# Optimization experiments

Measured on AMD Instinct MI355X. Metric: run time of the kernel, lower is better.

Reference implementation:

```python
import jax, jax.numpy as jnp
import numpy as np

HIDDEN = 1024


def setup_inputs() -> dict:
    key = jax.random.key(0)
    ks = jax.random.split(key, 9)
    B, S, Kq, H = 16, 4096, 64, HIDDEN
    scale = 1.0 / np.sqrt(H)
    return {
        "queries": jax.random.normal(ks[0], (B, Kq, H), jnp.float32),
        "keys": jax.random.normal(ks[1], (B, S, H), jnp.float32),
        "values": jax.random.normal(ks[2], (B, S, H), jnp.float32),
        "Wq": jax.random.normal(ks[3], (H, H), jnp.float32) * scale,
        "bq": jax.random.normal(ks[4], (H,), jnp.float32) * 0.02,
        "Wk": jax.random.normal(ks[5], (H, H), jnp.float32) * scale,
        "bk": jax.random.normal(ks[6], (H,), jnp.float32) * 0.02,
        "Wv": jax.random.normal(ks[7], (H, H), jnp.float32) * scale,
        "bv": jax.random.normal(ks[8], (H,), jnp.float32) * 0.02,
    }


def reference(queries, keys, values, Wq, bq, Wk, bk, Wv, bv):
    H = Wq.shape[0]
    scaling = jax.lax.rsqrt(jnp.asarray(H, queries.dtype))
    # torch Linear: x @ W^T + b
    q = queries @ Wq.T + bq            # (B, Kq, H)
    k = keys @ Wk.T + bk               # (B, S, H)
    v = values @ Wv.T + bv             # (B, S, H)
    # scores: k @ q^T -> (B, S, Kq), softmax over seq_len axis (dim=1)
    scores = jnp.einsum('bsh,bqh->bsq', k, q) * scaling
    attention_weights = jax.nn.softmax(scores, axis=1)
    # context: attn^T @ v -> (B, Kq, H)
    context = jnp.einsum('bsq,bsh->bqh', attention_weights, v)
    return context, attention_weights
```

## Files before the change

kernel.cpp:

```cpp
#include <hip/hip_runtime.h>
#include <hip/hip_bf16.h>

#define H 1024
#define SEQ 4096
#define BQ 64
#define NB 16

typedef float f32x4 __attribute__((ext_vector_type(4)));
typedef __bf16 bf16x8 __attribute__((ext_vector_type(8)));

__device__ __forceinline__ void split_bf16(const float* x, bf16x8& hi, bf16x8& lo)
{
    #pragma unroll
    for (int i = 0; i < 8; ++i) {
        float v = x[i];
        __bf16 h = (__bf16)v;
        hi[i] = h;
        lo[i] = (__bf16)(v - (float)h);
    }
}

__device__ __forceinline__ void gload_lds16(const float* g, void* lds)
{
    __builtin_amdgcn_global_load_lds(
        (const __attribute__((address_space(1))) void*)g,
        (__attribute__((address_space(3))) void*)lds, 16, 0, 0);
}

template<bool CVEC>
__global__ __launch_bounds__(512)
void gemm_bt_512(const float* __restrict__ A, const float* __restrict__ Bm,
                 const float* __restrict__ bias, float* __restrict__ C,
                 float scale, const float* __restrict__ bk,
                 float* __restrict__ cvec, float cscale)
{
    const int m0 = blockIdx.x * 64;
    const int n0 = blockIdx.y * 64;
    const int t   = threadIdx.x;
    const int w   = t >> 6;
    const int wm  = w & 3;
    const int kh  = w >> 2;
    const int l   = t & 63;
    const int row = l & 15;
    const int kg  = l >> 4;

    const float* ap = A + (size_t)(m0 + wm * 16 + row) * H + kh * 512 + kg * 8;
    const float* bp = Bm + (size_t)(n0 + row) * H + kh * 512 + kg * 8;

    f32x4 acc[4] = {};
    for (int k0 = 0; k0 < 512; k0 += 32) {
        float a8[8];
        *reinterpret_cast<float4*>(&a8[0]) = *reinterpret_cast<const float4*>(ap + k0);
        *reinterpret_cast<float4*>(&a8[4]) = *reinterpret_cast<const float4*>(ap + k0 + 4);
        bf16x8 ahi, alo;
        split_bf16(a8, ahi, alo);
        #pragma unroll
        for (int j = 0; j < 4; ++j) {
            float b8[8];
            const float* bjp = bp + (size_t)j * 16 * H + k0;
            *reinterpret_cast<float4*>(&b8[0]) = *reinterpret_cast<const float4*>(bjp);
            *reinterpret_cast<float4*>(&b8[4]) = *reinterpret_cast<const float4*>(bjp + 4);
            bf16x8 bhi, blo;
            split_bf16(b8, bhi, blo);
            acc[j] = __builtin_amdgcn_mfma_f32_16x16x32_bf16(ahi, bhi, acc[j], 0, 0, 0);
            acc[j] = __builtin_amdgcn_mfma_f32_16x16x32_bf16(ahi, blo, acc[j], 0, 0, 0);
            acc[j] = __builtin_amdgcn_mfma_f32_16x16x32_bf16(alo, bhi, acc[j], 0, 0, 0);
        }
    }

    __shared__ f32x4 red[4][4][64];
    if (kh == 1) {
        #pragma unroll
        for (int j = 0; j < 4; ++j) red[wm][j][l] = acc[j];
    }
    __syncthreads();
    if (kh == 0) {
        float p[4] = {0.f, 0.f, 0.f, 0.f};
        #pragma unroll
        for (int j = 0; j < 4; ++j) {
            f32x4 s = acc[j] + red[wm][j][l];
            int n = n0 + j * 16 + row;
            float bb = bias ? bias[n] : 0.f;
            float bkv = CVEC ? bk[n] : 0.f;
            #pragma unroll
            for (int r = 0; r < 4; ++r) {
                int m = m0 + wm * 16 + kg * 4 + r;
                float o = s[r] * scale + bb;
                C[(size_t)m * H + n] = o;
                if (CVEC) p[r] += o * bkv;
            }
        }
        if (CVEC) {
            #pragma unroll
            for (int r = 0; r < 4; ++r) {
                #pragma unroll
                for (int off = 1; off < 16; off <<= 1)
                    p[r] += __shfl_xor(p[r], off);
            }
            if (row == 0) {
                #pragma unroll
                for (int r = 0; r < 4; ++r)
                    atomicAdd(&cvec[m0 + wm * 16 + kg * 4 + r], p[r] * cscale);
            }
        }
    }
}

__global__ __launch_bounds__(512)
void ngemm_direct(const float* __restrict__ A, const float* __restrict__ Wk,
                  __bf16* __restrict__ Nhi, __bf16* __restrict__ Nlo, float scale)
{
    const int m0 = blockIdx.x * 64;
    const int n0 = blockIdx.y * 64;
    const int t   = threadIdx.x;
    const int w   = t >> 6;
    const int wm  = w & 3;
    const int kh  = w >> 2;
    const int l   = t & 63;
    const int row = l & 15;
    const int kg  = l >> 4;

    const float* ap = A + (size_t)(m0 + wm * 16 + row) * H + kh * 512 + kg * 8;
    const float* bp = Wk + (size_t)(kh * 512 + kg * 8) * H + n0 + row;

    f32x4 acc[4] = {};
    for (int k0 = 0; k0 < 512; k0 += 32) {
        float a8[8];
        *reinterpret_cast<float4*>(&a8[0]) = *reinterpret_cast<const float4*>(ap + k0);
        *reinterpret_cast<float4*>(&a8[4]) = *reinterpret_cast<const float4*>(ap + k0 + 4);
        bf16x8 ahi, alo;
        split_bf16(a8, ahi, alo);
        #pragma unroll
        for (int j = 0; j < 4; ++j) {
            float b8[8];
            #pragma unroll
            for (int e = 0; e < 8; ++e)
                b8[e] = bp[(size_t)(k0 + e) * H + j * 16];
            bf16x8 bhi, blo;
            split_bf16(b8, bhi, blo);
            acc[j] = __builtin_amdgcn_mfma_f32_16x16x32_bf16(ahi, bhi, acc[j], 0, 0, 0);
            acc[j] = __builtin_amdgcn_mfma_f32_16x16x32_bf16(ahi, blo, acc[j], 0, 0, 0);
            acc[j] = __builtin_amdgcn_mfma_f32_16x16x32_bf16(alo, bhi, acc[j], 0, 0, 0);
        }
    }

    __shared__ f32x4 red[4][4][64];
    if (kh == 1) {
        #pragma unroll
        for (int j = 0; j < 4; ++j) red[wm][j][l] = acc[j];
    }
    __syncthreads();
    if (kh == 0) {
        #pragma unroll
        for (int j = 0; j < 4; ++j) {
            f32x4 s = acc[j] + red[wm][j][l];
            int n = n0 + j * 16 + row;
            #pragma unroll
            for (int r = 0; r < 4; ++r) {
                int m = m0 + wm * 16 + kg * 4 + r;
                float v = s[r] * scale;
                __bf16 hi = (__bf16)v;
                Nhi[(size_t)m * H + n] = hi;
                Nlo[(size_t)m * H + n] = (__bf16)(v - (float)hi);
            }
        }
    }
}

__global__ __launch_bounds__(512, 4)
void scores_mfma(const float* __restrict__ keys,
                 const __bf16* __restrict__ Nhi, const __bf16* __restrict__ Nlo,
                 const float* __restrict__ cvec, float* __restrict__ scores,
                 float* __restrict__ pmax, float* __restrict__ psum)
{
    const int id = blockIdx.x;
    const int x  = id & 7;
    const int m  = id >> 3;
    const int b  = 2 * x + (m >> 5);
    const int ch = m & 31;
    const int s0 = ch * 128;

    const int t   = threadIdx.x;
    const int w   = t >> 6;
    const int l   = t & 63;
    const int row = l & 15;
    const int kg  = l >> 4;

    __shared__ __bf16 nshH[2][64][8][8];
    __shared__ __bf16 nshL[2][64][8][8];
    __shared__ float redm[8][64];

    const float* ka = keys + ((size_t)b * SEQ + s0 + w * 16 + row) * H + kg * 8;
    const __bf16* nhb = Nhi + (size_t)b * BQ * H;
    const __bf16* nlb = Nlo + (size_t)b * BQ * H;

    const int sqi = t >> 3;
    const int skb = t & 7;
    const int ssl = skb ^ (sqi & 7);

    float4 kr[2][4];
    bf16x8 nh[2], nl[2];
    #pragma unroll
    for (int ii = 0; ii < 2; ++ii) {
        kr[0][2 * ii + 0] = *reinterpret_cast<const float4*>(ka + ii * 32);
        kr[0][2 * ii + 1] = *reinterpret_cast<const float4*>(ka + ii * 32 + 4);
    }
    {
        size_t go = (size_t)sqi * H + skb * 8;
        nh[0] = *reinterpret_cast<const bf16x8*>(nhb + go);
        nl[0] = *reinterpret_cast<const bf16x8*>(nlb + go);
    }

    f32x4 acc[4] = {};
    #pragma unroll
    for (int c = 0; c < 16; ++c) {
        const int buf = c & 1;
        *reinterpret_cast<bf16x8*>(&nshH[buf][sqi][ssl][0]) = nh[buf];
        *reinterpret_cast<bf16x8*>(&nshL[buf][sqi][ssl][0]) = nl[buf];
        __syncthreads();
        if (c < 15) {
            const int kc = (c + 1) * 64;
            #pragma unroll
            for (int ii = 0; ii < 2; ++ii) {
                kr[buf ^ 1][2 * ii + 0] = *reinterpret_cast<const float4*>(ka + kc + ii * 32);
                kr[buf ^ 1][2 * ii + 1] = *reinterpret_cast<const float4*>(ka + kc + ii * 32 + 4);
            }
            size_t go = (size_t)sqi * H + kc + skb * 8;
            nh[buf ^ 1] = *reinterpret_cast<const bf16x8*>(nhb + go);
            nl[buf ^ 1] = *reinterpret_cast<const bf16x8*>(nlb + go);
        }
        #pragma unroll
        for (int ii = 0; ii < 2; ++ii) {
            float a8[8];
            *reinterpret_cast<float4*>(&a8[0]) = kr[buf][2 * ii + 0];
            *reinterpret_cast<float4*>(&a8[4]) = kr[buf][2 * ii + 1];
            bf16x8 ahi, alo;
            split_bf16(a8, ahi, alo);
            const int kb = ii * 4 + kg;
            const int slot = kb ^ (row & 7);
            #pragma unroll
            for (int j = 0; j < 4; ++j) {
                const int qi = j * 16 + row;
                bf16x8 bhi = *reinterpret_cast<const bf16x8*>(&nshH[buf][qi][slot][0]);
                bf16x8 blo = *reinterpret_cast<const bf16x8*>(&nshL[buf][qi][slot][0]);
                acc[j] = __builtin_amdgcn_mfma_f32_16x16x32_bf16(ahi, bhi, acc[j], 0, 0, 0);
                acc[j] = __builtin_amdgcn_mfma_f32_16x16x32_bf16(ahi, blo, acc[j], 0, 0, 0);
                acc[j] = __builtin_amdgcn_mfma_f32_16x16x32_bf16(alo, bhi, acc[j], 0, 0, 0);
            }
        }
    }

    #pragma unroll
    for (int j = 0; j < 4; ++j) {
        int qi = j * 16 + row;
        float cv = cvec[b * BQ + qi];
        #pragma unroll
        for (int r = 0; r < 4; ++r) {
            acc[j][r] += cv;
            int s = s0 + w * 16 + kg * 4 + r;
            scores[((size_t)b * SEQ + s) * BQ + qi] = acc[j][r];
        }
    }
    float mj[4];
    #pragma unroll
    for (int j = 0; j < 4; ++j) {
        float mm = fmaxf(fmaxf(acc[j][0], acc[j][1]), fmaxf(acc[j][2], acc[j][3]));
        mm = fmaxf(mm, __shfl_xor(mm, 16));
        mm = fmaxf(mm, __shfl_xor(mm, 32));
        mj[j] = mm;
    }
    __syncthreads();
    if (kg == 0) {
        #pragma unroll
        for (int j = 0; j < 4; ++j) redm[w][j * 16 + row] = mj[j];
    }
    __syncthreads();
    float Mj[4];
    #pragma unroll
    for (int j = 0; j < 4; ++j) {
        const int qi = j * 16 + row;
        float M = redm[0][qi];
        #pragma unroll
        for (int ww = 1; ww < 8; ++ww) M = fmaxf(M, redm[ww][qi]);
        Mj[j] = M;
    }
    float sj[4];
    #pragma unroll
    for (int j = 0; j < 4; ++j) {
        float s = 0.f;
        #pragma unroll
        for (int r = 0; r < 4; ++r) s += __expf(acc[j][r] - Mj[j]);
        s += __shfl_xor(s, 16);
        s += __shfl_xor(s, 32);
        sj[j] = s;
    }
    __syncthreads();
    if (kg == 0) {
        #pragma unroll
        for (int j = 0; j < 4; ++j) redm[w][j * 16 + row] = sj[j];
    }
    __syncthreads();
    if (w == 0 && kg == 0) {
        #pragma unroll
        for (int j = 0; j < 4; ++j) {
            const int qi = j * 16 + row;
            float ss = 0.f;
            #pragma unroll
            for (int ww = 0; ww < 8; ++ww) ss += redm[ww][qi];
            pmax[((size_t)b * 32 + ch) * 64 + qi] = Mj[j];
            psum[((size_t)b * 32 + ch) * 64 + qi] = ss;
        }
    }
}

__global__ __launch_bounds__(256)
void sm_norm(float* __restrict__ attn, const float* __restrict__ pmax,
             const float* __restrict__ psum, __hip_bfloat16* __restrict__ abfT)
{
    __shared__ float tile[64][133];
    const int b  = blockIdx.y;
    const int ch = blockIdx.x;
    const int t  = threadIdx.x;
    const int qi = t & 63;
    const int g  = t >> 6;

    float M = -1e30f;
    #pragma unroll 4
    for (int c = 0; c < 32; ++c)
        M = fmaxf(M, pmax[((size_t)b * 32 + c) * 64 + qi]);
    float ssum = 0.f;
    #pragma unroll 4
    for (int c = 0; c < 32; ++c)
        ssum += psum[((size_t)b * 32 + c) * 64 + qi] *
                __expf(pmax[((size_t)b * 32 + c) * 64 + qi] - M);
    const float inv = 1.f / ssum;

    float* sb = attn + ((size_t)b * SEQ + ch * 128) * BQ;
    #pragma unroll 8
    for (int i = 0; i < 32; ++i) {
        int sl = g + i * 4;
        size_t idx = (size_t)sl * BQ + qi;
        float w = __expf(sb[idx] - M) * inv;
        sb[idx] = w;
        tile[qi][sl] = w;
    }
    __syncthreads();
    const int qo = t >> 2;
    const int c  = (t & 3) * 32;
    __hip_bfloat16* dst = abfT + ((size_t)(b * BQ + qo)) * SEQ + ch * 128 + c;
    #pragma unroll
    for (int v = 0; v < 4; ++v) {
        bf16x8 w8;
        #pragma unroll
        for (int e = 0; e < 8; ++e)
            w8[e] = (__bf16)tile[qo][c + v * 8 + e];
        *reinterpret_cast<bf16x8*>(dst + v * 8) = w8;
    }
}

template<int SC>
__global__ __launch_bounds__(256)
void tmat_mfma(const __hip_bfloat16* __restrict__ abfT,
               const float* __restrict__ values,
               float* __restrict__ Tpart)
{
    const int i  = blockIdx.x;
    const int h0 = ((i >> 3) & 7) * 128;
    const int g  = (i & 7) + 8 * (i >> 6);
    const int b  = g / SC;
    const int sc = g % SC;
    const int schunk = SEQ / SC;

    const int w   = threadIdx.x >> 6;
    const int l   = threadIdx.x & 63;
    const int row = l & 15;
    const int kg  = l >> 4;
    const int sbase = sc * schunk;

    __shared__ float vlds[2][32][128];

    const __hip_bfloat16* ap = abfT + ((size_t)b * BQ + row) * SEQ + sbase + kg * 8;
    const float* vb = values + ((size_t)b * SEQ + sbase) * H + h0;

    const int nk = schunk / 32;

    #define STAGE(buf, k0)                                                     \
        {                                                                      \
            _Pragma("unroll")                                                  \
            for (int ii = 0; ii < 4; ++ii) {                                   \
                int elem = w * 1024 + ii * 256 + l * 4;                        \
                int k    = elem >> 7;                                          \
                int cc   = elem & 127;                                         \
                int csw  = cc ^ ((k >> 3) << 4);                               \
                const float* src = vb + (size_t)((k0) + k) * H + csw;          \
                gload_lds16(src, (void*)(&vlds[buf][0][0] + w * 1024 + ii * 256)); \
            }                                                                  \
        }

    f32x4 acc[4][2] = {};
    STAGE(0, 0);
    __syncthreads();

    for (int ks = 0; ks < nk; ++ks) {
        const int buf = ks & 1;
        if (ks + 1 < nk) STAGE(buf ^ 1, (ks + 1) * 32);
        const int k0 = ks * 32;
        bf16x8 a[4];
        #pragma unroll
        for (int q = 0; q < 4; ++q)
            a[q] = *reinterpret_cast<const bf16x8*>(ap + (size_t)q * 16 * SEQ + k0);
        #pragma unroll
        for (int j = 0; j < 2; ++j) {
            const int col = (w * 32 + j * 16 + row) ^ (kg << 4);
            float b8[8];
            #pragma unroll
            for (int e = 0; e < 8; ++e)
                b8[e] = vlds[buf][kg * 8 + e][col];
            bf16x8 bhi, blo;
            split_bf16(b8, bhi, blo);
            #pragma unroll
            for (int q = 0; q < 4; ++q) {
                acc[q][j] = __builtin_amdgcn_mfma_f32_16x16x32_bf16(a[q], bhi, acc[q][j], 0, 0, 0);
                acc[q][j] = __builtin_amdgcn_mfma_f32_16x16x32_bf16(a[q], blo, acc[q][j], 0, 0, 0);
            }
        }
        __syncthreads();
    }
    #undef STAGE

    float* tp = Tpart + ((size_t)sc * NB + b) * BQ * H;
    #pragma unroll
    for (int q = 0; q < 4; ++q) {
        #pragma unroll
        for (int j = 0; j < 2; ++j) {
            int h = h0 + w * 32 + j * 16 + row;
            #pragma unroll
            for (int r = 0; r < 4; ++r) {
                int qi = q * 16 + kg * 4 + r;
                tp[(size_t)qi * H + h] = acc[q][j][r];
            }
        }
    }
}

template<int SC>
__global__ __launch_bounds__(256)
void tsum_kernel(float* __restrict__ Tpart)
{
    const size_t stride = (size_t)NB * BQ * H;
    size_t i = ((size_t)blockIdx.x * 256 + threadIdx.x) * 4;
    f32x4 s = *reinterpret_cast<const f32x4*>(Tpart + i);
    #pragma unroll
    for (int p = 1; p < SC; ++p)
        s += *reinterpret_cast<const f32x4*>(Tpart + p * stride + i);
    *reinterpret_cast<f32x4*>(Tpart + i) = s;
}

extern "C" void kernel_launch(void* const* d_in, const int* in_sizes, int n_in,
                              void* d_out, int out_size, void* d_ws, size_t ws_size,
                              hipStream_t stream)
{
    const float* queries = (const float*)d_in[0];
    const float* keys    = (const float*)d_in[1];
    const float* values  = (const float*)d_in[2];
    const float* Wq = (const float*)d_in[3];
    const float* bq = (const float*)d_in[4];
    const float* Wk = (const float*)d_in[5];
    const float* bk = (const float*)d_in[6];
    const float* Wv = (const float*)d_in[7];
    const float* bv = (const float*)d_in[8];

    float* out     = (float*)d_out;
    float* context = out;
    float* attn    = out + (size_t)NB * BQ * H;

    const int SC = (ws_size >= (41ull << 20)) ? 8 : 2;

    char* ws = (char*)d_ws;
    float* q     = (float*)ws;
    __bf16* Nhi  = (__bf16*)(ws + (8ull << 20));
    __bf16* Nlo  = (__bf16*)(ws + (10ull << 20));
    float* Tpart = (float*)ws;
    __hip_bfloat16* abfT = (__hip_bfloat16*)(ws + (size_t)SC * (4ull << 20));
    char* smalls = ws + (size_t)SC * (4ull << 20) + (8ull << 20);
    float* cvec  = (float*)smalls;
    float* pmax  = (float*)(smalls + (128u << 10));
    float* psum  = (float*)(smalls + (512u << 10));

    const float scale = 0.03125f;

    hipMemsetAsync(cvec, 0, (size_t)NB * BQ * sizeof(float), stream);
    gemm_bt_512<true><<<dim3(16, 16), 512, 0, stream>>>(
        queries, Wq, bq, q, 1.0f, bk, cvec, scale);
    ngemm_direct<<<dim3(16, 16), 512, 0, stream>>>(q, Wk, Nhi, Nlo, scale);
    scores_mfma<<<512, 512, 0, stream>>>(keys, Nhi, Nlo, cvec, attn, pmax, psum);
    sm_norm<<<dim3(32, NB), 256, 0, stream>>>(attn, pmax, psum, abfT);
    if (SC == 8) tmat_mfma<8><<<8 * NB * 8, 256, 0, stream>>>(abfT, values, Tpart);
    else         tmat_mfma<2><<<8 * NB * 2, 256, 0, stream>>>(abfT, values, Tpart);
    if (SC == 8) tsum_kernel<8><<<1024, 256, 0, stream>>>(Tpart);
    else         tsum_kernel<2><<<1024, 256, 0, stream>>>(Tpart);
    gemm_bt_512<false><<<dim3(16, 16), 512, 0, stream>>>(
        Tpart, Wv, bv, context, 1.0f, nullptr, nullptr, 0.f);
}
```

Measured before the change: 281.8 us.

## Restructure scores kernel: async-stage keys to LDS, read split N from global

The scores kernel now uses 256-thread blocks over 64-row sequence chunks, doubling the grid and the number of partial softmax statistics. Key tiles are staged into a swizzled LDS double buffer with direct global-to-LDS loads. The bf16 hi/lo query-projection operands are read straight from global/L2 instead of through LDS, and the MFMA operand roles are swapped so keys become the B operand. The reduction is rewritten to use shuffles within a 16-lane group, and sm_norm now combines 64 partial chunks. The aim is to remove register staging of fp32 keys and the LDS traffic for N, at the cost of more partial stats and repeated global reads of N.

```diff
diff --git a/kernel.cpp b/kernel.cpp
--- a/kernel.cpp
+++ b/kernel.cpp
@@ -167,7 +167,7 @@
     }
 }
 
-__global__ __launch_bounds__(512, 4)
+__global__ __launch_bounds__(256)
 void scores_mfma(const float* __restrict__ keys,
                  const __bf16* __restrict__ Nhi, const __bf16* __restrict__ Nlo,
                  const float* __restrict__ cvec, float* __restrict__ scores,
@@ -176,139 +176,144 @@
     const int id = blockIdx.x;
     const int x  = id & 7;
     const int m  = id >> 3;
-    const int b  = 2 * x + (m >> 5);
-    const int ch = m & 31;
-    const int s0 = ch * 128;
+    const int b  = 2 * x + (m >> 6);
+    const int ch = m & 63;
+    const int s0 = ch * 64;
 
     const int t   = threadIdx.x;
     const int w   = t >> 6;
     const int l   = t & 63;
-    const int row = l & 15;
+    const int cl  = l & 15;
     const int kg  = l >> 4;
 
-    __shared__ __bf16 nshH[2][64][8][8];
-    __shared__ __bf16 nshL[2][64][8][8];
-    __shared__ float redm[8][64];
-
-    const float* ka = keys + ((size_t)b * SEQ + s0 + w * 16 + row) * H + kg * 8;
+    __shared__ float klds[2][64][8][8];
+    __shared__ float redm[4][64];
+
+    const float* kb_ = keys + ((size_t)b * SEQ + s0) * H;
     const __bf16* nhb = Nhi + (size_t)b * BQ * H;
     const __bf16* nlb = Nlo + (size_t)b * BQ * H;
 
-    const int sqi = t >> 3;
-    const int skb = t & 7;
-    const int ssl = skb ^ (sqi & 7);
-
-    float4 kr[2][4];
-    bf16x8 nh[2], nl[2];
-    #pragma unroll
-    for (int ii = 0; ii < 2; ++ii) {
-        kr[0][2 * ii + 0] = *reinterpret_cast<const float4*>(ka + ii * 32);
-        kr[0][2 * ii + 1] = *reinterpret_cast<const float4*>(ka + ii * 32 + 4);
-    }
-    {
-        size_t go = (size_t)sqi * H + skb * 8;
-        nh[0] = *reinterpret_cast<const bf16x8*>(nhb + go);
-        nl[0] = *reinterpret_cast<const bf16x8*>(nlb + go);
+    #define KSTAGE(buf, kc)                                                    \
+    {                                                                          \
+        _Pragma("unroll")                                                      \
+        for (int rd = 0; rd < 4; ++rd) {                                       \
+            int d  = rd * 1024 + w * 256 + l * 4;                              \
+            int ss = d >> 6;                                                   \
+            int sl = (d >> 3) & 7;                                             \
+            int e0 = d & 7;                                                    \
+            const float* src = kb_ + (size_t)ss * H + (kc) +                   \
+                               ((sl ^ (ss & 7)) << 3) + e0;                    \
+            gload_lds16(src, (void*)(&klds[buf][0][0][0] + rd * 1024 + w * 256)); \
+        }                                                                      \
     }
 
     f32x4 acc[4] = {};
-    #pragma unroll
+    KSTAGE(0, 0);
+    __syncthreads();
+
     for (int c = 0; c < 16; ++c) {
         const int buf = c & 1;
-        *reinterpret_cast<bf16x8*>(&nshH[buf][sqi][ssl][0]) = nh[buf];
-        *reinterpret_cast<bf16x8*>(&nshL[buf][sqi][ssl][0]) = nl[buf];
-        __syncthreads();
-        if (c < 15) {
-            const int kc = (c + 1) * 64;
-            #pragma unroll
-            for (int ii = 0; ii < 2; ++ii) {
-                kr[buf ^ 1][2 * ii + 0] = *reinterpret_cast<const float4*>(ka + kc + ii * 32);
-                kr[buf ^ 1][2 * ii + 1] = *reinterpret_cast<const float4*>(ka + kc + ii * 32 + 4);
-            }
-            size_t go = (size_t)sqi * H + kc + skb * 8;
-            nh[buf ^ 1] = *reinterpret_cast<const bf16x8*>(nhb + go);
-            nl[buf ^ 1] = *reinterpret_cast<const bf16x8*>(nlb + go);
-        }
+        if (c < 15) KSTAGE(buf ^ 1, (c + 1) * 64);
+        const int kc = c * 64;
         #pragma unroll
         for (int ii = 0; ii < 2; ++ii) {
-            float a8[8];
-            *reinterpret_cast<float4*>(&a8[0]) = kr[buf][2 * ii + 0];
-            *reinterpret_cast<float4*>(&a8[4]) = kr[buf][2 * ii + 1];
-            bf16x8 ahi, alo;
-            split_bf16(a8, ahi, alo);
-            const int kb = ii * 4 + kg;
-            const int slot = kb ^ (row & 7);
+            const int srow = w * 16 + cl;
+            const int slot = (ii * 4 + kg) ^ (srow & 7);
+            float b8[8];
+            *reinterpret_cast<float4*>(&b8[0]) =
+                *reinterpret_cast<const float4*>(&klds[buf][srow][slot][0]);
+            *reinterpret_cast<float4*>(&b8[4]) =
+                *reinterpret_cast<const float4*>(&klds[buf][srow][slot][4]);
+            bf16x8 bhi, blo;
+            split_bf16(b8, bhi, blo);
             #pragma unroll
             for (int j = 0; j < 4; ++j) {
-                const int qi = j * 16 + row;
-                bf16x8 bhi = *reinterpret_cast<const bf16x8*>(&nshH[buf][qi][slot][0]);
-                bf16x8 blo = *reinterpret_cast<const bf16x8*>(&nshL[buf][qi][slot][0]);
+                size_t ao = (size_t)(j * 16 + cl) * H + kc + ii * 32 + kg * 8;
+                bf16x8 ahi = *reinterpret_cast<const bf16x8*>(nhb + ao);
+                bf16x8 alo = *reinterpret_cast<const bf16x8*>(nlb + ao);
                 acc[j] = __builtin_amdgcn_mfma_f32_16x16x32_bf16(ahi, bhi, acc[j], 0, 0, 0);
                 acc[j] = __builtin_amdgcn_mfma_f32_16x16x32_bf16(ahi, blo, acc[j], 0, 0, 0);
                 acc[j] = __builtin_amdgcn_mfma_f32_16x16x32_bf16(alo, bhi, acc[j], 0, 0, 0);
             }
         }
-    }
-
+        __syncthreads();
+    }
+    #undef KSTAGE
+
+    const int s = s0 + w * 16 + cl;
+    f32x4 cvr[4];
+    #pragma unroll
+    for (int j = 0; j < 4; ++j)
+        cvr[j] = *reinterpret_cast<const f32x4*>(&cvec[b * BQ + j * 16 + kg * 4]);
     #pragma unroll
     for (int j = 0; j < 4; ++j) {
-        int qi = j * 16 + row;
-        float cv = cvec[b * BQ + qi];
         #pragma unroll
         for (int r = 0; r < 4; ++r) {
-            acc[j][r] += cv;
-            int s = s0 + w * 16 + kg * 4 + r;
-            scores[((size_t)b * SEQ + s) * BQ + qi] = acc[j][r];
-        }
-    }
-    float mj[4];
+            float v = acc[j][r] + cvr[j][r];
+            acc[j][r] = v;
+            scores[((size_t)b * SEQ + s) * BQ + j * 16 + kg * 4 + r] = v;
+        }
+    }
+    f32x4 mm[4];
     #pragma unroll
     for (int j = 0; j < 4; ++j) {
-        float mm = fmaxf(fmaxf(acc[j][0], acc[j][1]), fmaxf(acc[j][2], acc[j][3]));
-        mm = fmaxf(mm, __shfl_xor(mm, 16));
-        mm = fmaxf(mm, __shfl_xor(mm, 32));
-        mj[j] = mm;
-    }
-    __syncthreads();
-    if (kg == 0) {
-        #pragma unroll
-        for (int j = 0; j < 4; ++j) redm[w][j * 16 + row] = mj[j];
-    }
-    __syncthreads();
-    float Mj[4];
+        mm[j] = acc[j];
+        #pragma unroll
+        for (int off = 1; off < 16; off <<= 1) {
+            #pragma unroll
+            for (int r = 0; r < 4; ++r)
+                mm[j][r] = fmaxf(mm[j][r], __shfl_xor(mm[j][r], off));
+        }
+    }
+    if (cl == 0) {
+        #pragma unroll
+        for (int j = 0; j < 4; ++j)
+            *reinterpret_cast<f32x4*>(&redm[w][j * 16 + kg * 4]) = mm[j];
+    }
+    __syncthreads();
+    f32x4 Mj[4];
     #pragma unroll
     for (int j = 0; j < 4; ++j) {
-        const int qi = j * 16 + row;
-        float M = redm[0][qi];
-        #pragma unroll
-        for (int ww = 1; ww < 8; ++ww) M = fmaxf(M, redm[ww][qi]);
+        f32x4 M = *reinterpret_cast<const f32x4*>(&redm[0][j * 16 + kg * 4]);
+        #pragma unroll
+        for (int ww = 1; ww < 4; ++ww) {
+            f32x4 o = *reinterpret_cast<const f32x4*>(&redm[ww][j * 16 + kg * 4]);
+            #pragma unroll
+            for (int r = 0; r < 4; ++r) M[r] = fmaxf(M[r], o[r]);
+        }
         Mj[j] = M;
     }
-    float sj[4];
+    __syncthreads();
+    f32x4 se[4];
     #pragma unroll
     for (int j = 0; j < 4; ++j) {
-        float s = 0.f;
-        #pragma unroll
-        for (int r = 0; r < 4; ++r) s += __expf(acc[j][r] - Mj[j]);
-        s += __shfl_xor(s, 16);
-        s += __shfl_xor(s, 32);
-        sj[j] = s;
-    }
-    __syncthreads();
-    if (kg == 0) {
-        #pragma unroll
-        for (int j = 0; j < 4; ++j) redm[w][j * 16 + row] = sj[j];
-    }
-    __syncthreads();
-    if (w == 0 && kg == 0) {
+        #pragma unroll
+        for (int r = 0; r < 4; ++r) se[j][r] = __expf(acc[j][r] - Mj[j][r]);
+        #pragma unroll
+        for (int off = 1; off < 16; off <<= 1) {
+            #pragma unroll
+            for (int r = 0; r < 4; ++r)
+                se[j][r] += __shfl_xor(se[j][r], off);
+        }
+    }
+    if (cl == 0) {
+        #pragma unroll
+        for (int j = 0; j < 4; ++j)
+            *reinterpret_cast<f32x4*>(&redm[w][j * 16 + kg * 4]) = se[j];
+    }
+    __syncthreads();
+    if (w == 0 && cl == 0) {
         #pragma unroll
         for (int j = 0; j < 4; ++j) {
-            const int qi = j * 16 + row;
-            float ss = 0.f;
-            #pragma unroll
-            for (int ww = 0; ww < 8; ++ww) ss += redm[ww][qi];
-            pmax[((size_t)b * 32 + ch) * 64 + qi] = Mj[j];
-            psum[((size_t)b * 32 + ch) * 64 + qi] = ss;
+            f32x4 ssum = *reinterpret_cast<const f32x4*>(&redm[0][j * 16 + kg * 4]);
+            #pragma unroll
+            for (int ww = 1; ww < 4; ++ww) {
+                f32x4 o = *reinterpret_cast<const f32x4*>(&redm[ww][j * 16 + kg * 4]);
+                #pragma unroll
+                for (int r = 0; r < 4; ++r) ssum[r] += o[r];
+            }
+            *reinterpret_cast<f32x4*>(&pmax[((size_t)b * 64 + ch) * 64 + j * 16 + kg * 4]) = Mj[j];
+            *reinterpret_cast<f32x4*>(&psum[((size_t)b * 64 + ch) * 64 + j * 16 + kg * 4]) = ssum;
         }
     }
 }
@@ -326,13 +331,13 @@
 
     float M = -1e30f;
     #pragma unroll 4
-    for (int c = 0; c < 32; ++c)
-        M = fmaxf(M, pmax[((size_t)b * 32 + c) * 64 + qi]);
+    for (int c = 0; c < 64; ++c)
+        M = fmaxf(M, pmax[((size_t)b * 64 + c) * 64 + qi]);
     float ssum = 0.f;
     #pragma unroll 4
-    for (int c = 0; c < 32; ++c)
-        ssum += psum[((size_t)b * 32 + c) * 64 + qi] *
-                __expf(pmax[((size_t)b * 32 + c) * 64 + qi] - M);
+    for (int c = 0; c < 64; ++c)
+        ssum += psum[((size_t)b * 64 + c) * 64 + qi] *
+                __expf(pmax[((size_t)b * 64 + c) * 64 + qi] - M);
     const float inv = 1.f / ssum;
 
     float* sb = attn + ((size_t)b * SEQ + ch * 128) * BQ;
@@ -493,7 +498,7 @@
     gemm_bt_512<true><<<dim3(16, 16), 512, 0, stream>>>(
         queries, Wq, bq, q, 1.0f, bk, cvec, scale);
     ngemm_direct<<<dim3(16, 16), 512, 0, stream>>>(q, Wk, Nhi, Nlo, scale);
-    scores_mfma<<<512, 512, 0, stream>>>(keys, Nhi, Nlo, cvec, attn, pmax, psum);
+    scores_mfma<<<1024, 256, 0, stream>>>(keys, Nhi, Nlo, cvec, attn, pmax, psum);
     sm_norm<<<dim3(32, NB), 256, 0, stream>>>(attn, pmax, psum, abfT);
     if (SC == 8) tmat_mfma<8><<<8 * NB * 8, 256, 0, stream>>>(abfT, values, Tpart);
     else         tmat_mfma<2><<<8 * NB * 2, 256, 0, stream>>>(abfT, values, Tpart);
```

Measured after the change: 359.7 us. 27.6% more time.

## Transpose Wk once and drop the keys low-part MFMA in scores

Applied to the files above, without the earlier changes.

Replaces the strided-load ngemm_direct with a small shared-memory transpose of Wk followed by the generic row-major gemm_bt_512, which now has a template mode that writes hi/lo bf16 outputs. In scores_mfma the keys are converted to a single bf16 instead of a hi/lo pair, removing one of three MFMAs per tile along with the split arithmetic. This lowers the compute in the dominant scores kernel and makes the N-matrix GEMM loads coalesced, at the cost of reduced precision on the keys operand and one extra launch.

```diff
diff --git a/kernel.cpp b/kernel.cpp
--- a/kernel.cpp
+++ b/kernel.cpp
@@ -20,6 +20,12 @@
     }
 }
 
+__device__ __forceinline__ void cvt_bf16(const float* x, bf16x8& hi)
+{
+    #pragma unroll
+    for (int i = 0; i < 8; ++i) hi[i] = (__bf16)x[i];
+}
+
 __device__ __forceinline__ void gload_lds16(const float* g, void* lds)
 {
     __builtin_amdgcn_global_load_lds(
@@ -27,12 +33,13 @@
         (__attribute__((address_space(3))) void*)lds, 16, 0, 0);
 }
 
-template<bool CVEC>
+template<bool CVEC, bool NOUT>
 __global__ __launch_bounds__(512)
 void gemm_bt_512(const float* __restrict__ A, const float* __restrict__ Bm,
                  const float* __restrict__ bias, float* __restrict__ C,
                  float scale, const float* __restrict__ bk,
-                 float* __restrict__ cvec, float cscale)
+                 float* __restrict__ cvec, float cscale,
+                 __bf16* __restrict__ Nhi, __bf16* __restrict__ Nlo)
 {
     const int m0 = blockIdx.x * 64;
     const int n0 = blockIdx.y * 64;
@@ -80,13 +87,19 @@
         for (int j = 0; j < 4; ++j) {
             f32x4 s = acc[j] + red[wm][j][l];
             int n = n0 + j * 16 + row;
-            float bb = bias ? bias[n] : 0.f;
+            float bb = (!NOUT && bias) ? bias[n] : 0.f;
             float bkv = CVEC ? bk[n] : 0.f;
             #pragma unroll
             for (int r = 0; r < 4; ++r) {
                 int m = m0 + wm * 16 + kg * 4 + r;
                 float o = s[r] * scale + bb;
-                C[(size_t)m * H + n] = o;
+                if (NOUT) {
+                    __bf16 hi = (__bf16)o;
+                    Nhi[(size_t)m * H + n] = hi;
+                    Nlo[(size_t)m * H + n] = (__bf16)(o - (float)hi);
+                } else {
+                    C[(size_t)m * H + n] = o;
+                }
                 if (CVEC) p[r] += o * bkv;
             }
         }
@@ -106,64 +119,33 @@
     }
 }
 
-__global__ __launch_bounds__(512)
-void ngemm_direct(const float* __restrict__ A, const float* __restrict__ Wk,
-                  __bf16* __restrict__ Nhi, __bf16* __restrict__ Nlo, float scale)
-{
-    const int m0 = blockIdx.x * 64;
+__global__ __launch_bounds__(256)
+void transpose_k(const float* __restrict__ Wk, float* __restrict__ WkT)
+{
+    __shared__ float tile[64][65];
+    const int k0 = blockIdx.x * 64;
     const int n0 = blockIdx.y * 64;
-    const int t   = threadIdx.x;
-    const int w   = t >> 6;
-    const int wm  = w & 3;
-    const int kh  = w >> 2;
-    const int l   = t & 63;
-    const int row = l & 15;
-    const int kg  = l >> 4;
-
-    const float* ap = A + (size_t)(m0 + wm * 16 + row) * H + kh * 512 + kg * 8;
-    const float* bp = Wk + (size_t)(kh * 512 + kg * 8) * H + n0 + row;
-
-    f32x4 acc[4] = {};
-    for (int k0 = 0; k0 < 512; k0 += 32) {
-        float a8[8];
-        *reinterpret_cast<float4*>(&a8[0]) = *reinterpret_cast<const float4*>(ap + k0);
-        *reinterpret_cast<float4*>(&a8[4]) = *reinterpret_cast<const float4*>(ap + k0 + 4);
-        bf16x8 ahi, alo;
-        split_bf16(a8, ahi, alo);
-        #pragma unroll
-        for (int j = 0; j < 4; ++j) {
-            float b8[8];
-            #pragma unroll
-            for (int e = 0; e < 8; ++e)
-                b8[e] = bp[(size_t)(k0 + e) * H + j * 16];
-            bf16x8 bhi, blo;
-            split_bf16(b8, bhi, blo);
-            acc[j] = __builtin_amdgcn_mfma_f32_16x16x32_bf16(ahi, bhi, acc[j], 0, 0, 0);
-            acc[j] = __builtin_amdgcn_mfma_f32_16x16x32_bf16(ahi, blo, acc[j], 0, 0, 0);
-            acc[j] = __builtin_amdgcn_mfma_f32_16x16x32_bf16(alo, bhi, acc[j], 0, 0, 0);
-        }
-    }
-
-    __shared__ f32x4 red[4][4][64];
-    if (kh == 1) {
-        #pragma unroll
-        for (int j = 0; j < 4; ++j) red[wm][j][l] = acc[j];
-    }
-    __syncthreads();
-    if (kh == 0) {
-        #pragma unroll
-        for (int j = 0; j < 4; ++j) {
-            f32x4 s = acc[j] + red[wm][j][l];
-            int n = n0 + j * 16 + row;
-            #pragma unroll
-            for (int r = 0; r < 4; ++r) {
-                int m = m0 + wm * 16 + kg * 4 + r;
-                float v = s[r] * scale;
-                __bf16 hi = (__bf16)v;
-                Nhi[(size_t)m * H + n] = hi;
-                Nlo[(size_t)m * H + n] = (__bf16)(v - (float)hi);
-            }
-        }
+    const int t  = threadIdx.x;
+    const int c4 = (t & 15) * 4;
+    const int r  = t >> 4;
+    #pragma unroll
+    for (int p = 0; p < 4; ++p) {
+        float4 v = *reinterpret_cast<const float4*>(&Wk[(size_t)(k0 + r + 16 * p) * H + n0 + c4]);
+        tile[r + 16 * p][c4 + 0] = v.x;
+        tile[r + 16 * p][c4 + 1] = v.y;
+        tile[r + 16 * p][c4 + 2] = v.z;
+        tile[r + 16 * p][c4 + 3] = v.w;
+    }
+    __syncthreads();
+    #pragma unroll
+    for (int p = 0; p < 4; ++p) {
+        int rr = r + 16 * p;
+        float4 o;
+        o.x = tile[c4 + 0][rr];
+        o.y = tile[c4 + 1][rr];
+        o.z = tile[c4 + 2][rr];
+        o.w = tile[c4 + 3][rr];
+        *reinterpret_cast<float4*>(&WkT[(size_t)(n0 + rr) * H + k0 + c4]) = o;
     }
 }
 
@@ -234,8 +216,8 @@
             float a8[8];
             *reinterpret_cast<float4*>(&a8[0]) = kr[buf][2 * ii + 0];
             *reinterpret_cast<float4*>(&a8[4]) = kr[buf][2 * ii + 1];
-            bf16x8 ahi, alo;
-            split_bf16(a8, ahi, alo);
+            bf16x8 ahi;
+            cvt_bf16(a8, ahi);
             const int kb = ii * 4 + kg;
             const int slot = kb ^ (row & 7);
             #pragma unroll
@@ -245,7 +227,6 @@
                 bf16x8 blo = *reinterpret_cast<const bf16x8*>(&nshL[buf][qi][slot][0]);
                 acc[j] = __builtin_amdgcn_mfma_f32_16x16x32_bf16(ahi, bhi, acc[j], 0, 0, 0);
                 acc[j] = __builtin_amdgcn_mfma_f32_16x16x32_bf16(ahi, blo, acc[j], 0, 0, 0);
-                acc[j] = __builtin_amdgcn_mfma_f32_16x16x32_bf16(alo, bhi, acc[j], 0, 0, 0);
             }
         }
     }
@@ -478,6 +459,7 @@
 
     char* ws = (char*)d_ws;
     float* q     = (float*)ws;
+    float* WkT   = (float*)(ws + (4ull << 20));
     __bf16* Nhi  = (__bf16*)(ws + (8ull << 20));
     __bf16* Nlo  = (__bf16*)(ws + (10ull << 20));
     float* Tpart = (float*)ws;
@@ -490,15 +472,17 @@
     const float scale = 0.03125f;
 
     hipMemsetAsync(cvec, 0, (size_t)NB * BQ * sizeof(float), stream);
-    gemm_bt_512<true><<<dim3(16, 16), 512, 0, stream>>>(
-        queries, Wq, bq, q, 1.0f, bk, cvec, scale);
-    ngemm_direct<<<dim3(16, 16), 512, 0, stream>>>(q, Wk, Nhi, Nlo, scale);
+    transpose_k<<<dim3(16, 16), 256, 0, stream>>>(Wk, WkT);
+    gemm_bt_512<true, false><<<dim3(16, 16), 512, 0, stream>>>(
+        queries, Wq, bq, q, 1.0f, bk, cvec, scale, nullptr, nullptr);
+    gemm_bt_512<false, true><<<dim3(16, 16), 512, 0, stream>>>(
+        q, WkT, nullptr, nullptr, scale, nullptr, nullptr, 0.f, Nhi, Nlo);
     scores_mfma<<<512, 512, 0, stream>>>(keys, Nhi, Nlo, cvec, attn, pmax, psum);
     sm_norm<<<dim3(32, NB), 256, 0, stream>>>(attn, pmax, psum, abfT);
     if (SC == 8) tmat_mfma<8><<<8 * NB * 8, 256, 0, stream>>>(abfT, values, Tpart);
     else         tmat_mfma<2><<<8 * NB * 2, 256, 0, stream>>>(abfT, values, Tpart);
     if (SC == 8) tsum_kernel<8><<<1024, 256, 0, stream>>>(Tpart);
     else         tsum_kernel<2><<<1024, 256, 0, stream>>>(Tpart);
-    gemm_bt_512<false><<<dim3(16, 16), 512, 0, stream>>>(
-        Tpart, Wv, bv, context, 1.0f, nullptr, nullptr, 0.f);
-}
+    gemm_bt_512<false, false><<<dim3(16, 16), 512, 0, stream>>>(
+        Tpart, Wv, bv, context, 1.0f, nullptr, nullptr, 0.f, nullptr, nullptr);
+}
```

Measured after the change: 299.1 us. +6.1%, slower.

## Triple-buffer tmat_mfma loads and stage attention weights through LDS

Applied to the files above, without the earlier changes.

The value-times-attention kernel moves from a double-buffered to a triple-buffered LDS pipeline with two tiles in flight. It uses explicit vmcnt waits and raw barriers in place of __syncthreads. The bf16 attention operand, previously read directly from global memory into registers, is now staged into LDS with async global-to-LDS loads alongside the values. This is meant to hide global latency better, at the cost of more LDS per block (which may reduce occupancy) and hand-tuned wait counts that must match the number of issued loads.

```diff
diff --git a/kernel.cpp b/kernel.cpp
--- a/kernel.cpp
+++ b/kernel.cpp
@@ -20,7 +20,7 @@
     }
 }
 
-__device__ __forceinline__ void gload_lds16(const float* g, void* lds)
+__device__ __forceinline__ void gload_lds16(const void* g, void* lds)
 {
     __builtin_amdgcn_global_load_lds(
         (const __attribute__((address_space(1))) void*)g,
@@ -364,12 +364,14 @@
                const float* __restrict__ values,
                float* __restrict__ Tpart)
 {
+    constexpr int schunk = SEQ / SC;
+    constexpr int nk = schunk / 32;
+
     const int i  = blockIdx.x;
     const int h0 = ((i >> 3) & 7) * 128;
     const int g  = (i & 7) + 8 * (i >> 6);
     const int b  = g / SC;
     const int sc = g % SC;
-    const int schunk = SEQ / SC;
 
     const int w   = threadIdx.x >> 6;
     const int l   = threadIdx.x & 63;
@@ -377,14 +379,13 @@
     const int kg  = l >> 4;
     const int sbase = sc * schunk;
 
-    __shared__ float vlds[2][32][128];
-
-    const __hip_bfloat16* ap = abfT + ((size_t)b * BQ + row) * SEQ + sbase + kg * 8;
+    __shared__ float vlds[3][32][128];
+    __shared__ __hip_bfloat16 alds[3][64][32];
+
+    const __hip_bfloat16* ab = abfT + (size_t)b * BQ * SEQ + sbase;
     const float* vb = values + ((size_t)b * SEQ + sbase) * H + h0;
 
-    const int nk = schunk / 32;
-
-    #define STAGE(buf, k0)                                                     \
+    #define VSTAGE(buf, c)                                                     \
         {                                                                      \
             _Pragma("unroll")                                                  \
             for (int ii = 0; ii < 4; ++ii) {                                   \
@@ -392,23 +393,41 @@
                 int k    = elem >> 7;                                          \
                 int cc   = elem & 127;                                         \
                 int csw  = cc ^ ((k >> 3) << 4);                               \
-                const float* src = vb + (size_t)((k0) + k) * H + csw;          \
+                const float* src = vb + (size_t)((c) * 32 + k) * H + csw;      \
                 gload_lds16(src, (void*)(&vlds[buf][0][0] + w * 1024 + ii * 256)); \
             }                                                                  \
         }
+    #define ASTAGE(buf, c)                                                     \
+        {                                                                      \
+            int aqi = w * 16 + (l >> 2);                                       \
+            const __hip_bfloat16* srcA =                                       \
+                ab + (size_t)aqi * SEQ + (c) * 32 + (l & 3) * 8;               \
+            gload_lds16(srcA, (void*)(&alds[buf][0][0] + w * 512));            \
+        }
 
     f32x4 acc[4][2] = {};
-    STAGE(0, 0);
-    __syncthreads();
+    ASTAGE(0, 0); VSTAGE(0, 0);
+    ASTAGE(1, 1); VSTAGE(1, 1);
 
     for (int ks = 0; ks < nk; ++ks) {
-        const int buf = ks & 1;
-        if (ks + 1 < nk) STAGE(buf ^ 1, (ks + 1) * 32);
-        const int k0 = ks * 32;
+        const int buf = ks % 3;
+        if (ks + 2 < nk) {
+            const int nb2 = (ks + 2) % 3;
+            ASTAGE(nb2, ks + 2); VSTAGE(nb2, ks + 2);
+            asm volatile("s_waitcnt vmcnt(10)" ::: "memory");
+        } else if (ks + 1 < nk) {
+            asm volatile("s_waitcnt vmcnt(5)" ::: "memory");
+        } else {
+            asm volatile("s_waitcnt vmcnt(0)" ::: "memory");
+        }
+        __builtin_amdgcn_sched_barrier(0);
+        __builtin_amdgcn_s_barrier();
+        __builtin_amdgcn_sched_barrier(0);
+
         bf16x8 a[4];
         #pragma unroll
         for (int q = 0; q < 4; ++q)
-            a[q] = *reinterpret_cast<const bf16x8*>(ap + (size_t)q * 16 * SEQ + k0);
+            a[q] = *reinterpret_cast<const bf16x8*>(&alds[buf][q * 16 + row][kg * 8]);
         #pragma unroll
         for (int j = 0; j < 2; ++j) {
             const int col = (w * 32 + j * 16 + row) ^ (kg << 4);
@@ -424,9 +443,12 @@
                 acc[q][j] = __builtin_amdgcn_mfma_f32_16x16x32_bf16(a[q], blo, acc[q][j], 0, 0, 0);
             }
         }
-        __syncthreads();
-    }
-    #undef STAGE
+        __builtin_amdgcn_sched_barrier(0);
+        __builtin_amdgcn_s_barrier();
+        __builtin_amdgcn_sched_barrier(0);
+    }
+    #undef VSTAGE
+    #undef ASTAGE
 
     float* tp = Tpart + ((size_t)sc * NB + b) * BQ * H;
     #pragma unroll
```

Measured after the change: 277.7 us. About the same (-1.5%).
